# Kernel optimization log

Hardware: AMD Instinct MI355X
Metric: run time of the kernel (lower is better)

## Reference

```python
import jax, jax.numpy as jnp
import numpy as np

N_HEAD = 16
NUM_EXPERTS = 8
TOP_K = 2
LN_EPS = 1e-5


def setup_inputs() -> dict:
    key = jax.random.key(0)
    B, T, D = 8, 1024, 1024
    H = 4 * D
    E = NUM_EXPERTS
    ks = jax.random.split(key, 24)
    s = 0.02
    inp = {
        "x": jax.random.normal(ks[0], (B, T, D), jnp.float32),
        "ln1_g": jnp.ones((D,), jnp.float32),
        "ln1_b": jnp.zeros((D,), jnp.float32),
        "ln2_g": jnp.ones((D,), jnp.float32),
        "ln2_b": jnp.zeros((D,), jnp.float32),
        "Wq": jax.random.normal(ks[1], (D, D), jnp.float32) * s,
        "bq": jnp.zeros((D,), jnp.float32),
        "Wk": jax.random.normal(ks[2], (D, D), jnp.float32) * s,
        "bk": jnp.zeros((D,), jnp.float32),
        "Wv": jax.random.normal(ks[3], (D, D), jnp.float32) * s,
        "bv": jnp.zeros((D,), jnp.float32),
        "Wp": jax.random.normal(ks[4], (D, D), jnp.float32) * s,
        "bp": jnp.zeros((D,), jnp.float32),
        "gate_W": jax.random.normal(ks[5], (D, E), jnp.float32) * s,
        "gate_b": jnp.zeros((E,), jnp.float32),
        "exp_W1": jax.random.normal(ks[6], (E, D, H), jnp.float32) * s,
        "exp_b1": jnp.zeros((E, H), jnp.float32),
        "exp_W2": jax.random.normal(ks[7], (E, H, D), jnp.float32) * s,
        "exp_b2": jnp.zeros((E, D), jnp.float32),
    }
    return inp


def _layernorm(x, g, b):
    mu = jnp.mean(x, axis=-1, keepdims=True)
    var = jnp.mean(jnp.square(x - mu), axis=-1, keepdims=True)
    return (x - mu) * jax.lax.rsqrt(var + LN_EPS) * g + b


def _attention(h, Wq, bq, Wk, bk, Wv, bv, Wp, bp):
    B, T, D = h.shape
    hd = D // N_HEAD
    # [B,T,D] -> [B,Hh,T,hd]
    def split(z):
        return z.reshape(B, T, N_HEAD, hd).transpose(0, 2, 1, 3)
    q = split(h @ Wq + bq)
    k = split(h @ Wk + bk)
    v = split(h @ Wv + bv)
    att = jnp.einsum('bhqd,bhkd->bhqk', q, k) / jnp.sqrt(jnp.float32(hd))
    causal = jnp.tril(jnp.ones((T, T), bool))
    att = jnp.where(causal, att, -jnp.inf)
    att = jax.nn.softmax(att, axis=-1)
    y = jnp.einsum('bhqk,bhkd->bhqd', att, v)
    y = y.transpose(0, 2, 1, 3).reshape(B, T, D)
    return y @ Wp + bp


def _token_moe(h, gate_W, gate_b, exp_W1, exp_b1, exp_W2, exp_b2):
    B, T, D = h.shape
    flat = h.reshape(-1, D)                      # [N, D]
    N = flat.shape[0]
    logits = flat @ gate_W + gate_b              # [N, E]
    top_v, top_i = jax.lax.top_k(logits, TOP_K)  # [N, k]
    w = jax.nn.softmax(top_v, axis=-1)           # [N, k]
    # scatter top-k weights into dense [N, E] combine weights
    w_full = jnp.zeros((N, NUM_EXPERTS), flat.dtype)
    w_full = w_full.at[jnp.arange(N)[:, None], top_i].add(w)
    out = jnp.zeros_like(flat)
    for e in range(NUM_EXPERTS):  # small fixed expert count
        mid = jax.nn.gelu(flat @ exp_W1[e] + exp_b1[e], approximate=False)
        y_e = mid @ exp_W2[e] + exp_b2[e]
        out = out + w_full[:, e:e + 1] * y_e
    return out.reshape(B, T, D)


def reference(x, ln1_g, ln1_b, ln2_g, ln2_b, Wq, bq, Wk, bk, Wv, bv, Wp, bp,
              gate_W, gate_b, exp_W1, exp_b1, exp_W2, exp_b2):
    x = x + _attention(_layernorm(x, ln1_g, ln1_b), Wq, bq, Wk, bk, Wv, bv, Wp, bp)
    x = x + _token_moe(_layernorm(x, ln2_g, ln2_b), gate_W, gate_b,
                       exp_W1, exp_b1, exp_W2, exp_b2)
    return x
```

## Files before the change

kernel.cpp:

```cpp
#include <hip/hip_runtime.h>
#include <hip/hip_bf16.h>

#define D_MODEL 1024
#define H_MLP   4096
#define N_TOK   8192
#define T_SEQ   1024
#define NHEADS  16
#define HEAD_D  64
#define NEXPERT 8
#define LN_EPS  1e-5f
#define MAX_TILES 136
#define MAX_ROWS  (MAX_TILES * 128)
#define MB (1024 * 1024)

using f32x4 = __attribute__((ext_vector_type(4))) float;
using bh8   = __attribute__((ext_vector_type(8))) short;
typedef _Float16 h8 __attribute__((ext_vector_type(8)));

__device__ __forceinline__ unsigned short f2b(float f) {
  unsigned u = __float_as_uint(f);
  return (unsigned short)((u + 0x7FFFu + ((u >> 16) & 1u)) >> 16);
}
__device__ __forceinline__ float b2f(unsigned short h) {
  return __uint_as_float(((unsigned)h) << 16);
}
__device__ __forceinline__ void split16(float v, unsigned short& hi, unsigned short& lo) {
  const _Float16 h = (_Float16)v;
  const _Float16 l = (_Float16)(v - (float)h);
  hi = __builtin_bit_cast(unsigned short, h);
  lo = __builtin_bit_cast(unsigned short, l);
}
__device__ __forceinline__ void gll16(const unsigned short* g, unsigned short* lds) {
  __builtin_amdgcn_global_load_lds(
      (const __attribute__((address_space(1))) unsigned int*)(const void*)g,
      (__attribute__((address_space(3))) unsigned int*)(void*)lds, 16, 0, 0);
}

__global__ __launch_bounds__(256) void ln1_kernel(
    const float* __restrict__ x, const float* __restrict__ g,
    const float* __restrict__ b, unsigned short* __restrict__ oh,
    unsigned short* __restrict__ ol) {
  const int t = blockIdx.x, tid = threadIdx.x;
  const float4 v = ((const float4*)(x + (size_t)t * D_MODEL))[tid];
  float s  = v.x + v.y + v.z + v.w;
  float sq = v.x * v.x + v.y * v.y + v.z * v.z + v.w * v.w;
  __shared__ float red[8];
  #pragma unroll
  for (int o = 32; o > 0; o >>= 1) { s += __shfl_down(s, o); sq += __shfl_down(sq, o); }
  if ((tid & 63) == 0) { red[tid >> 6] = s; red[4 + (tid >> 6)] = sq; }
  __syncthreads();
  s  = red[0] + red[1] + red[2] + red[3];
  sq = red[4] + red[5] + red[6] + red[7];
  const float mu = s * (1.0f / D_MODEL);
  const float var = sq * (1.0f / D_MODEL) - mu * mu;
  const float rs = 1.0f / sqrtf(var + LN_EPS);
  const float4 gv = ((const float4*)g)[tid];
  const float4 bv = ((const float4*)b)[tid];
  float4 o;
  o.x = (v.x - mu) * rs * gv.x + bv.x;
  o.y = (v.y - mu) * rs * gv.y + bv.y;
  o.z = (v.z - mu) * rs * gv.z + bv.z;
  o.w = (v.w - mu) * rs * gv.w + bv.w;
  ushort4 hs, ls;
  split16(o.x, hs.x, ls.x); split16(o.y, hs.y, ls.y);
  split16(o.z, hs.z, ls.z); split16(o.w, hs.w, ls.w);
  ((ushort4*)(oh + (size_t)t * D_MODEL))[tid] = hs;
  ((ushort4*)(ol + (size_t)t * D_MODEL))[tid] = ls;
}

template<int MODE>
__global__ __launch_bounds__(256) void gemm_split_kernel(
    const unsigned short* __restrict__ Ah_g, const unsigned short* __restrict__ Al_g,
    const unsigned short* __restrict__ Bh_g, const unsigned short* __restrict__ Bl_g,
    const float* __restrict__ bias, const float* __restrict__ Rres,
    unsigned short* __restrict__ Ch, unsigned short* __restrict__ Cl,
    float* __restrict__ Cf, int M, int N, int K) {
  __shared__ unsigned short LAh[128 * 32], LAl[128 * 32];
  __shared__ unsigned short LBh[128 * 32], LBl[128 * 32];
  const int tid = threadIdx.x, lane = tid & 63, w = tid >> 6;
  const int bm = blockIdx.x * 128, bn = blockIdx.y * 128;
  const int wm = (w >> 1) * 64, wn = (w & 1) * 64;
  f32x4 acc[4][4];
  #pragma unroll
  for (int i = 0; i < 4; ++i)
    #pragma unroll
    for (int j = 0; j < 4; ++j) acc[i][j] = (f32x4){0.f, 0.f, 0.f, 0.f};
  const int lrow16 = lane >> 2, kq8 = (lane & 3) << 3;
  const int r0 = w * 16 + lrow16, r1 = 64 + w * 16 + lrow16;
  const size_t a0 = (size_t)(bm + r0) * K + kq8, a1 = (size_t)(bm + r1) * K + kq8;
  const size_t b0 = (size_t)(bn + r0) * K + kq8, b1 = (size_t)(bn + r1) * K + kq8;
  const int lb0 = (w * 16) * 32, lb1 = (64 + w * 16) * 32;
  const int lrow = lane & 15, lk = (lane >> 4) << 3;
  for (int k0 = 0; k0 < K; k0 += 32) {
    gll16(Ah_g + a0 + k0, &LAh[lb0]); gll16(Ah_g + a1 + k0, &LAh[lb1]);
    gll16(Al_g + a0 + k0, &LAl[lb0]); gll16(Al_g + a1 + k0, &LAl[lb1]);
    gll16(Bh_g + b0 + k0, &LBh[lb0]); gll16(Bh_g + b1 + k0, &LBh[lb1]);
    gll16(Bl_g + b0 + k0, &LBl[lb0]); gll16(Bl_g + b1 + k0, &LBl[lb1]);
    __syncthreads();
    h8 ah[4], al[4], bh[4], bl[4];
    #pragma unroll
    for (int i = 0; i < 4; ++i) {
      ah[i] = *(const h8*)&LAh[(wm + i * 16 + lrow) * 32 + lk];
      al[i] = *(const h8*)&LAl[(wm + i * 16 + lrow) * 32 + lk];
    }
    #pragma unroll
    for (int j = 0; j < 4; ++j) {
      bh[j] = *(const h8*)&LBh[(wn + j * 16 + lrow) * 32 + lk];
      bl[j] = *(const h8*)&LBl[(wn + j * 16 + lrow) * 32 + lk];
    }
    #pragma unroll
    for (int i = 0; i < 4; ++i)
      #pragma unroll
      for (int j = 0; j < 4; ++j) {
        acc[i][j] = __builtin_amdgcn_mfma_f32_16x16x32_f16(ah[i], bh[j], acc[i][j], 0, 0, 0);
        acc[i][j] = __builtin_amdgcn_mfma_f32_16x16x32_f16(ah[i], bl[j], acc[i][j], 0, 0, 0);
        acc[i][j] = __builtin_amdgcn_mfma_f32_16x16x32_f16(al[i], bh[j], acc[i][j], 0, 0, 0);
      }
    __syncthreads();
  }
  const int lc = lane & 15, lr4 = (lane >> 4) * 4;
  #pragma unroll
  for (int i = 0; i < 4; ++i)
    #pragma unroll
    for (int j = 0; j < 4; ++j) {
      const int col = bn + wn + j * 16 + lc;
      const float bsv = bias[col];
      #pragma unroll
      for (int qq = 0; qq < 4; ++qq) {
        const size_t row = (size_t)bm + wm + i * 16 + lr4 + qq;
        const size_t idx = row * N + col;
        const float v = acc[i][j][qq] + bsv;
        if (MODE == 0) {
          unsigned short hi, lo;
          split16(v, hi, lo);
          Ch[idx] = hi; Cl[idx] = lo;
        } else {
          Cf[idx] = v + Rres[idx];
        }
      }
    }
}

__global__ __launch_bounds__(256) void vtrans_kernel(
    const unsigned short* __restrict__ src, unsigned short* __restrict__ dst) {
  __shared__ unsigned short tile[64][72];
  const int tid = threadIdx.x;
  const int t0 = blockIdx.x * 64, bh = blockIdx.y;
  const int b = bh >> 4, h = bh & 15;
  #pragma unroll
  for (int it = 0; it < 2; ++it) {
    const int sg = tid + it * 256;
    const int r = sg >> 3, s = sg & 7;
    *(uint4*)&tile[r][s * 8] =
        *(const uint4*)(src + ((size_t)b * T_SEQ + t0 + r) * D_MODEL + h * HEAD_D + s * 8);
  }
  __syncthreads();
  #pragma unroll
  for (int it = 0; it < 2; ++it) {
    const int sg = tid + it * 256;
    const int d = sg >> 3, s = sg & 7;
    unsigned short v8[8] __attribute__((aligned(16)));
    #pragma unroll
    for (int j = 0; j < 8; ++j) v8[j] = tile[s * 8 + j][d];
    *(uint4*)(dst + ((size_t)bh * HEAD_D + d) * T_SEQ + t0 + s * 8) = *(const uint4*)v8;
  }
}

__global__ __launch_bounds__(256) void attn_mfma_kernel(
    const unsigned short* __restrict__ qh_g, const unsigned short* __restrict__ ql_g,
    const unsigned short* __restrict__ kh_g, const unsigned short* __restrict__ kl_g,
    const unsigned short* __restrict__ vth_g, const unsigned short* __restrict__ vtl_g,
    unsigned short* __restrict__ yh, unsigned short* __restrict__ yl) {
  __shared__ unsigned short Kh[64][72], Kl[64][72], Vh[64][72], Vl[64][72];
  __shared__ float Ps[4][16][68];
  const int tid = threadIdx.x, lane = tid & 63, w = tid >> 6;
  const int g = lane >> 4, c = lane & 15;
  const int qt = blockIdx.x, bh = blockIdx.y, b = bh >> 4, h = bh & 15;
  const size_t qrow0 = (size_t)b * T_SEQ + qt * 64;
  h8 aqh[2], aql[2];
  {
    const size_t rq = (qrow0 + w * 16 + c) * D_MODEL + h * HEAD_D + g * 8;
    aqh[0] = *(const h8*)(qh_g + rq);
    aqh[1] = *(const h8*)(qh_g + rq + 32);
    aql[0] = *(const h8*)(ql_g + rq);
    aql[1] = *(const h8*)(ql_g + rq + 32);
  }
  f32x4 oacc[4];
  #pragma unroll
  for (int i = 0; i < 4; ++i) oacc[i] = (f32x4){0.f, 0.f, 0.f, 0.f};
  float m[4] = {-3e38f, -3e38f, -3e38f, -3e38f};
  float l[4] = {0.f, 0.f, 0.f, 0.f};
  const int sgr = tid >> 3, sgs = tid & 7;
  for (int kt = 0; kt <= qt; ++kt) {
    const int kv0 = kt * 64;
    __syncthreads();
    {
      const size_t kb = ((size_t)b * T_SEQ + kv0) * D_MODEL + h * HEAD_D + sgs * 8;
      const size_t vb = (size_t)bh * HEAD_D * T_SEQ + kv0 + sgs * 8;
      *(uint4*)&Kh[sgr][sgs * 8]      = *(const uint4*)(kh_g + kb + (size_t)sgr * D_MODEL);
      *(uint4*)&Kh[sgr + 32][sgs * 8] = *(const uint4*)(kh_g + kb + (size_t)(sgr + 32) * D_MODEL);
      *(uint4*)&Kl[sgr][sgs * 8]      = *(const uint4*)(kl_g + kb + (size_t)sgr * D_MODEL);
      *(uint4*)&Kl[sgr + 32][sgs * 8] = *(const uint4*)(kl_g + kb + (size_t)(sgr + 32) * D_MODEL);
      *(uint4*)&Vh[sgr][sgs * 8]      = *(const uint4*)(vth_g + vb + (size_t)sgr * T_SEQ);
      *(uint4*)&Vh[sgr + 32][sgs * 8] = *(const uint4*)(vth_g + vb + (size_t)(sgr + 32) * T_SEQ);
      *(uint4*)&Vl[sgr][sgs * 8]      = *(const uint4*)(vtl_g + vb + (size_t)sgr * T_SEQ);
      *(uint4*)&Vl[sgr + 32][sgs * 8] = *(const uint4*)(vtl_g + vb + (size_t)(sgr + 32) * T_SEQ);
    }
    __syncthreads();
    f32x4 sv[4];
    #pragma unroll
    for (int nt = 0; nt < 4; ++nt) {
      f32x4 s = {0.f, 0.f, 0.f, 0.f};
      #pragma unroll
      for (int ks = 0; ks < 2; ++ks) {
        const h8 bkh = *(const h8*)&Kh[nt * 16 + c][ks * 32 + g * 8];
        const h8 bkl = *(const h8*)&Kl[nt * 16 + c][ks * 32 + g * 8];
        s = __builtin_amdgcn_mfma_f32_16x16x32_f16(aqh[ks], bkh, s, 0, 0, 0);
        s = __builtin_amdgcn_mfma_f32_16x16x32_f16(aqh[ks], bkl, s, 0, 0, 0);
        s = __builtin_amdgcn_mfma_f32_16x16x32_f16(aql[ks], bkh, s, 0, 0, 0);
      }
      sv[nt] = s;
    }
    float pm[4] = {-3e38f, -3e38f, -3e38f, -3e38f};
    #pragma unroll
    for (int nt = 0; nt < 4; ++nt)
      #pragma unroll
      for (int qq = 0; qq < 4; ++qq) {
        float sval = sv[nt][qq] * 0.125f;
        const int krow = kv0 + nt * 16 + c;
        const int qrow = qt * 64 + w * 16 + g * 4 + qq;
        sval = (krow <= qrow) ? sval : -3.0e38f;
        sv[nt][qq] = sval;
        pm[qq] = fmaxf(pm[qq], sval);
      }
    #pragma unroll
    for (int o = 1; o < 16; o <<= 1)
      #pragma unroll
      for (int qq = 0; qq < 4; ++qq) pm[qq] = fmaxf(pm[qq], __shfl_xor(pm[qq], o));
    float psum[4];
    #pragma unroll
    for (int qq = 0; qq < 4; ++qq) {
      const float mnew = fmaxf(m[qq], pm[qq]);
      const float sc = expf(m[qq] - mnew);
      m[qq] = mnew;
      l[qq] *= sc;
      #pragma unroll
      for (int dt = 0; dt < 4; ++dt) oacc[dt][qq] *= sc;
      psum[qq] = 0.f;
    }
    #pragma unroll
    for (int nt = 0; nt < 4; ++nt)
      #pragma unroll
      for (int qq = 0; qq < 4; ++qq) {
        const float p = expf(sv[nt][qq] - m[qq]);
        Ps[w][g * 4 + qq][nt * 16 + c] = p;
        psum[qq] += p;
      }
    #pragma unroll
    for (int o = 1; o < 16; o <<= 1)
      #pragma unroll
      for (int qq = 0; qq < 4; ++qq) psum[qq] += __shfl_xor(psum[qq], o);
    #pragma unroll
    for (int qq = 0; qq < 4; ++qq) l[qq] += psum[qq];
    #pragma unroll
    for (int ks = 0; ks < 2; ++ks) {
      const float4 p0 = *(const float4*)&Ps[w][c][ks * 32 + g * 8];
      const float4 p1 = *(const float4*)&Ps[w][c][ks * 32 + g * 8 + 4];
      const float pv[8] = {p0.x, p0.y, p0.z, p0.w, p1.x, p1.y, p1.z, p1.w};
      h8 pah, pal;
      #pragma unroll
      for (int j = 0; j < 8; ++j) {
        const _Float16 hi = (_Float16)pv[j];
        pah[j] = hi;
        pal[j] = (_Float16)(pv[j] - (float)hi);
      }
      #pragma unroll
      for (int dt = 0; dt < 4; ++dt) {
        const h8 bvh = *(const h8*)&Vh[dt * 16 + c][ks * 32 + g * 8];
        const h8 bvl = *(const h8*)&Vl[dt * 16 + c][ks * 32 + g * 8];
        oacc[dt] = __builtin_amdgcn_mfma_f32_16x16x32_f16(pah, bvh, oacc[dt], 0, 0, 0);
        oacc[dt] = __builtin_amdgcn_mfma_f32_16x16x32_f16(pah, bvl, oacc[dt], 0, 0, 0);
        oacc[dt] = __builtin_amdgcn_mfma_f32_16x16x32_f16(pal, bvh, oacc[dt], 0, 0, 0);
      }
    }
  }
  #pragma unroll
  for (int qq = 0; qq < 4; ++qq) {
    const float inv = 1.0f / l[qq];
    const size_t row = (qrow0 + w * 16 + g * 4 + qq) * D_MODEL + h * HEAD_D;
    #pragma unroll
    for (int dt = 0; dt < 4; ++dt) {
      unsigned short hi, lo;
      split16(oacc[dt][qq] * inv, hi, lo);
      yh[row + dt * 16 + c] = hi;
      yl[row + dt * 16 + c] = lo;
    }
  }
}

__global__ __launch_bounds__(256) void ln2_route_kernel(
    const float* __restrict__ x1, const float* __restrict__ g,
    const float* __restrict__ b, const float* __restrict__ gW,
    const float* __restrict__ gb, unsigned short* __restrict__ h2b,
    int2* __restrict__ tok_e, float2* __restrict__ tok_w, int* __restrict__ counts) {
  const int t = blockIdx.x, tid = threadIdx.x;
  const float4 v = ((const float4*)(x1 + (size_t)t * D_MODEL))[tid];
  float s  = v.x + v.y + v.z + v.w;
  float sq = v.x * v.x + v.y * v.y + v.z * v.z + v.w * v.w;
  __shared__ float red[8];
  __shared__ float lred[4][8];
  #pragma unroll
  for (int o = 32; o > 0; o >>= 1) { s += __shfl_down(s, o); sq += __shfl_down(sq, o); }
  if ((tid & 63) == 0) { red[tid >> 6] = s; red[4 + (tid >> 6)] = sq; }
  __syncthreads();
  s  = red[0] + red[1] + red[2] + red[3];
  sq = red[4] + red[5] + red[6] + red[7];
  const float mu = s * (1.0f / D_MODEL);
  const float var = sq * (1.0f / D_MODEL) - mu * mu;
  const float rs = 1.0f / sqrtf(var + LN_EPS);
  const float4 gv = ((const float4*)g)[tid];
  const float4 bv = ((const float4*)b)[tid];
  float4 hv;
  hv.x = (v.x - mu) * rs * gv.x + bv.x;
  hv.y = (v.y - mu) * rs * gv.y + bv.y;
  hv.z = (v.z - mu) * rs * gv.z + bv.z;
  hv.w = (v.w - mu) * rs * gv.w + bv.w;
  ushort4 hs;
  hs.x = f2b(hv.x); hs.y = f2b(hv.y); hs.z = f2b(hv.z); hs.w = f2b(hv.w);
  ((ushort4*)(h2b + (size_t)t * D_MODEL))[tid] = hs;
  float lg[8];
  const float* gwr = gW + (size_t)tid * 32;
  #pragma unroll
  for (int e = 0; e < 8; ++e)
    lg[e] = hv.x * gwr[e] + hv.y * gwr[8 + e] +
            hv.z * gwr[16 + e] + hv.w * gwr[24 + e];
  #pragma unroll
  for (int o = 32; o > 0; o >>= 1)
    #pragma unroll
    for (int e = 0; e < 8; ++e) lg[e] += __shfl_down(lg[e], o);
  if ((tid & 63) == 0)
    #pragma unroll
    for (int e = 0; e < 8; ++e) lred[tid >> 6][e] = lg[e];
  __syncthreads();
  if (tid == 0) {
    float L[8];
    #pragma unroll
    for (int e = 0; e < 8; ++e)
      L[e] = lred[0][e] + lred[1][e] + lred[2][e] + lred[3][e] + gb[e];
    int e0 = 0; float v0 = L[0];
    for (int e = 1; e < 8; ++e) if (L[e] > v0) { v0 = L[e]; e0 = e; }
    int e1 = (e0 == 0) ? 1 : 0; float v1 = L[e1];
    for (int e = 0; e < 8; ++e) if (e != e0 && L[e] > v1) { v1 = L[e]; e1 = e; }
    const float ew = expf(v1 - v0);
    const float inv = 1.0f / (1.0f + ew);
    tok_e[t] = make_int2(e0, e1);
    tok_w[t] = make_float2(inv, ew * inv);
    atomicAdd(&counts[e0], 1);
    atomicAdd(&counts[e1], 1);
  }
}

__global__ void route_offsets_kernel(const int* __restrict__ counts, int* __restrict__ off_al,
    int* __restrict__ ntiles, int* __restrict__ map_e, int* __restrict__ map_row) {
  if (threadIdx.x != 0 || blockIdx.x != 0) return;
  int off = 0, ti = 0;
  for (int e = 0; e < NEXPERT; ++e) {
    off_al[e] = off;
    const int tiles = (counts[e] + 127) >> 7;
    for (int j = 0; j < tiles; ++j) { map_e[ti] = e; map_row[ti] = off + (j << 7); ++ti; }
    off += tiles << 7;
  }
  off_al[NEXPERT] = off;
  ntiles[0] = ti;
}

__global__ __launch_bounds__(256) void place_kernel(
    const int2* __restrict__ tok_e, const int* __restrict__ off_al,
    int* __restrict__ cursors, int* __restrict__ list, int2* __restrict__ tok_pos) {
  const int t = blockIdx.x * 256 + threadIdx.x;
  if (t >= N_TOK) return;
  const int2 te = tok_e[t];
  const int p0 = off_al[te.x] + atomicAdd(&cursors[te.x], 1);
  const int p1 = off_al[te.y] + atomicAdd(&cursors[te.y], 1);
  list[p0] = t; list[p1] = t;
  tok_pos[t] = make_int2(p0, p1);
}

__global__ __launch_bounds__(256) void fill_pad_kernel(
    const int* __restrict__ counts, const int* __restrict__ off_al, int* __restrict__ list) {
  const int i = blockIdx.x * 256 + threadIdx.x;
  const int e = i >> 7, j = i & 127;
  if (e >= NEXPERT) return;
  const int start = off_al[e] + counts[e];
  if (start + j < off_al[e + 1]) list[start + j] = 0;
}

__global__ void transpose_cvt_kernel(
    const float* __restrict__ in, unsigned short* __restrict__ outp, int R, int C) {
  __shared__ float tile[32][33];
  const int e = blockIdx.z;
  const float* I = in + (size_t)e * R * C;
  unsigned short* O = outp + (size_t)e * R * C;
  const int c0 = blockIdx.x * 32, r0 = blockIdx.y * 32;
  const int tx = threadIdx.x, ty = threadIdx.y;
  #pragma unroll
  for (int j = 0; j < 32; j += 8)
    tile[ty + j][tx] = I[(size_t)(r0 + ty + j) * C + c0 + tx];
  __syncthreads();
  #pragma unroll
  for (int j = 0; j < 32; j += 8)
    O[(size_t)(c0 + ty + j) * R + r0 + tx] = f2b(tile[tx][ty + j]);
}

__global__ void transpose_cvt_f16_kernel(
    const float* __restrict__ in, unsigned short* __restrict__ oh,
    unsigned short* __restrict__ ol, int R, int C) {
  __shared__ float tile[32][33];
  const int c0 = blockIdx.x * 32, r0 = blockIdx.y * 32;
  const int tx = threadIdx.x, ty = threadIdx.y;
  #pragma unroll
  for (int j = 0; j < 32; j += 8)
    tile[ty + j][tx] = in[(size_t)(r0 + ty + j) * C + c0 + tx];
  __syncthreads();
  #pragma unroll
  for (int j = 0; j < 32; j += 8) {
    unsigned short hi, lo;
    split16(tile[tx][ty + j], hi, lo);
    oh[(size_t)(c0 + ty + j) * R + r0 + tx] = hi;
    ol[(size_t)(c0 + ty + j) * R + r0 + tx] = lo;
  }
}

template<int GELU_OUT, int GATHER>
__global__ __launch_bounds__(256) void moe_gemm_kernel(
    const unsigned short* __restrict__ Abase, const unsigned short* __restrict__ Bbase,
    const float* __restrict__ biasBase, unsigned short* __restrict__ midOut,
    float* __restrict__ fOut, const int* __restrict__ list,
    const int* __restrict__ map_e, const int* __restrict__ map_row,
    const int* __restrict__ ntiles_p, int K, int N) {
  const int mt = blockIdx.x;
  if (mt >= ntiles_p[0]) return;
  const int e = map_e[mt];
  const int row0 = map_row[mt];
  const int bn = blockIdx.y * 128;
  const unsigned short* Bp = Bbase + (size_t)e * (size_t)N * (size_t)K;
  const float* bias = biasBase + (size_t)e * N;
  __shared__ unsigned short As[128 * 32];
  __shared__ unsigned short Bs[128 * 32];
  const int tid = threadIdx.x, lane = tid & 63, wid = tid >> 6;
  const int wm = (wid >> 1) * 64, wn = (wid & 1) * 64;
  f32x4 acc[4][4];
  #pragma unroll
  for (int i = 0; i < 4; ++i)
    #pragma unroll
    for (int j = 0; j < 4; ++j) acc[i][j] = (f32x4){0.f, 0.f, 0.f, 0.f};
  const int lrow16 = lane >> 2, kq8 = (lane & 3) << 3;
  const int r0 = wid * 16 + lrow16, r1 = 64 + wid * 16 + lrow16;
  size_t arow0, arow1;
  if (GATHER) {
    arow0 = (size_t)list[row0 + r0] * (size_t)K + kq8;
    arow1 = (size_t)list[row0 + r1] * (size_t)K + kq8;
  } else {
    arow0 = (size_t)(row0 + r0) * (size_t)K + kq8;
    arow1 = (size_t)(row0 + r1) * (size_t)K + kq8;
  }
  const size_t brow0 = (size_t)(bn + r0) * (size_t)K + kq8;
  const size_t brow1 = (size_t)(bn + r1) * (size_t)K + kq8;
  const int lb0 = (wid * 16) * 32, lb1 = (64 + wid * 16) * 32;
  const int lrow = lane & 15, lk = (lane >> 4) << 3;
  for (int k0 = 0; k0 < K; k0 += 32) {
    gll16(Abase + arow0 + k0, &As[lb0]);
    gll16(Abase + arow1 + k0, &As[lb1]);
    gll16(Bp + brow0 + k0, &Bs[lb0]);
    gll16(Bp + brow1 + k0, &Bs[lb1]);
    __syncthreads();
    bh8 a[4], b[4];
    #pragma unroll
    for (int i = 0; i < 4; ++i) a[i] = *(const bh8*)&As[(wm + i * 16 + lrow) * 32 + lk];
    #pragma unroll
    for (int j = 0; j < 4; ++j) b[j] = *(const bh8*)&Bs[(wn + j * 16 + lrow) * 32 + lk];
    #pragma unroll
    for (int i = 0; i < 4; ++i)
      #pragma unroll
      for (int j = 0; j < 4; ++j)
        acc[i][j] = __builtin_amdgcn_mfma_f32_16x16x32_bf16(a[i], b[j], acc[i][j], 0, 0, 0);
    __syncthreads();
  }
  const int lc = lane & 15, lr4 = (lane >> 4) * 4;
  #pragma unroll
  for (int i = 0; i < 4; ++i)
    #pragma unroll
    for (int j = 0; j < 4; ++j) {
      const int col = bn + wn + j * 16 + lc;
      const float bsv = bias[col];
      #pragma unroll
      for (int qq = 0; qq < 4; ++qq) {
        const int rowl = wm + i * 16 + lr4 + qq;
        const size_t idx = (size_t)(row0 + rowl) * N + col;
        const float xv = acc[i][j][qq] + bsv;
        if (GELU_OUT) {
          const float gel = 0.5f * xv * (1.0f + erff(xv * 0.70710678118654752f));
          midOut[idx] = f2b(gel);
        } else {
          fOut[idx] = xv;
        }
      }
    }
}

__global__ __launch_bounds__(256) void combine_kernel(
    const float* __restrict__ x1, const float* __restrict__ ylist,
    const int2* __restrict__ tok_pos, const float2* __restrict__ tok_w,
    float* __restrict__ outp) {
  const int t = blockIdx.x, tid = threadIdx.x;
  const int2 p = tok_pos[t];
  const float2 w = tok_w[t];
  const float4 a  = ((const float4*)(x1 + (size_t)t * D_MODEL))[tid];
  const float4 y0 = ((const float4*)(ylist + (size_t)p.x * D_MODEL))[tid];
  const float4 y1 = ((const float4*)(ylist + (size_t)p.y * D_MODEL))[tid];
  float4 o;
  o.x = a.x + w.x * y0.x + w.y * y1.x;
  o.y = a.y + w.x * y0.y + w.y * y1.y;
  o.z = a.z + w.x * y0.z + w.y * y1.z;
  o.w = a.w + w.x * y0.w + w.y * y1.w;
  ((float4*)(outp + (size_t)t * D_MODEL))[tid] = o;
}

extern "C" void kernel_launch(void* const* d_in, const int* in_sizes, int n_in,
                              void* d_out, int out_size, void* d_ws, size_t ws_size,
                              hipStream_t stream) {
  const float* x    = (const float*)d_in[0];
  const float* ln1g = (const float*)d_in[1];
  const float* ln1b = (const float*)d_in[2];
  const float* ln2g = (const float*)d_in[3];
  const float* ln2b = (const float*)d_in[4];
  const float* Wq   = (const float*)d_in[5];
  const float* bq   = (const float*)d_in[6];
  const float* Wk   = (const float*)d_in[7];
  const float* bk   = (const float*)d_in[8];
  const float* Wv   = (const float*)d_in[9];
  const float* bv   = (const float*)d_in[10];
  const float* Wp   = (const float*)d_in[11];
  const float* bp   = (const float*)d_in[12];
  const float* gW   = (const float*)d_in[13];
  const float* gb   = (const float*)d_in[14];
  const float* eW1  = (const float*)d_in[15];
  const float* eb1  = (const float*)d_in[16];
  const float* eW2  = (const float*)d_in[17];
  const float* eb2  = (const float*)d_in[18];
  float* out = (float*)d_out;
  (void)in_sizes; (void)n_in; (void)out_size;

  char* wsb = (char*)d_ws;
  size_t off = 0;
  auto alloc = [&](size_t bytes) -> void* {
    void* p = wsb + off;
    off += (bytes + 255) & ~(size_t)255;
    return p;
  };
  int*  counts  = (int*)alloc(32);
  int*  cursors = (int*)alloc(32);
  int*  off_al  = (int*)alloc(64);
  int*  ntiles  = (int*)alloc(64);
  int*  map_e   = (int*)alloc(MAX_TILES * 4);
  int*  map_row = (int*)alloc(MAX_TILES * 4);
  const size_t ctrl_bytes = off;
  int2*   tok_e   = (int2*)alloc((size_t)N_TOK * 8);
  float2* tok_w   = (float2*)alloc((size_t)N_TOK * 8);
  int2*   tok_pos = (int2*)alloc((size_t)N_TOK * 8);
  int*    list    = (int*)alloc((size_t)MAX_ROWS * 4);
  float* x1  = (float*)alloc((size_t)N_TOK * D_MODEL * 4);
  unsigned short* h2b = (unsigned short*)alloc((size_t)N_TOK * D_MODEL * 2);
  unsigned short* W1T = (unsigned short*)alloc((size_t)NEXPERT * D_MODEL * H_MLP * 2);
  unsigned short* W2T = (unsigned short*)alloc((size_t)NEXPERT * D_MODEL * H_MLP * 2);
  float* ylist = (float*)alloc((size_t)MAX_ROWS * D_MODEL * 4);
  unsigned short* WqTh = (unsigned short*)alloc((size_t)D_MODEL * D_MODEL * 2);
  unsigned short* WqTl = (unsigned short*)alloc((size_t)D_MODEL * D_MODEL * 2);
  unsigned short* WkTh = (unsigned short*)alloc((size_t)D_MODEL * D_MODEL * 2);
  unsigned short* WkTl = (unsigned short*)alloc((size_t)D_MODEL * D_MODEL * 2);
  unsigned short* WvTh = (unsigned short*)alloc((size_t)D_MODEL * D_MODEL * 2);
  unsigned short* WvTl = (unsigned short*)alloc((size_t)D_MODEL * D_MODEL * 2);
  unsigned short* WpTh = (unsigned short*)alloc((size_t)D_MODEL * D_MODEL * 2);
  unsigned short* WpTl = (unsigned short*)alloc((size_t)D_MODEL * D_MODEL * 2);
  char* arena = (char*)alloc((size_t)160 * MB);
  unsigned short* h1h = (unsigned short*)(arena);
  unsigned short* h1l = (unsigned short*)(arena + (size_t) 16 * MB);
  unsigned short* qh_ = (unsigned short*)(arena + (size_t) 32 * MB);
  unsigned short* ql_ = (unsigned short*)(arena + (size_t) 48 * MB);
  unsigned short* kh_ = (unsigned short*)(arena + (size_t) 64 * MB);
  unsigned short* kl_ = (unsigned short*)(arena + (size_t) 80 * MB);
  unsigned short* vh_ = (unsigned short*)(arena + (size_t) 96 * MB);
  unsigned short* vl_ = (unsigned short*)(arena + (size_t)112 * MB);
  unsigned short* vth_ = (unsigned short*)(arena + (size_t)128 * MB);
  unsigned short* vtl_ = (unsigned short*)(arena + (size_t)144 * MB);
  unsigned short* yh_ = vh_;
  unsigned short* yl_ = vl_;
  unsigned short* mid = (unsigned short*)(arena);
  if (off > ws_size) return;

  hipMemsetAsync(d_ws, 0, ctrl_bytes, stream);

  transpose_cvt_kernel<<<dim3(H_MLP / 32, D_MODEL / 32, NEXPERT), dim3(32, 8), 0, stream>>>(
      eW1, W1T, D_MODEL, H_MLP);
  transpose_cvt_kernel<<<dim3(D_MODEL / 32, H_MLP / 32, NEXPERT), dim3(32, 8), 0, stream>>>(
      eW2, W2T, H_MLP, D_MODEL);
  transpose_cvt_f16_kernel<<<dim3(32, 32), dim3(32, 8), 0, stream>>>(Wq, WqTh, WqTl, D_MODEL, D_MODEL);
  transpose_cvt_f16_kernel<<<dim3(32, 32), dim3(32, 8), 0, stream>>>(Wk, WkTh, WkTl, D_MODEL, D_MODEL);
  transpose_cvt_f16_kernel<<<dim3(32, 32), dim3(32, 8), 0, stream>>>(Wv, WvTh, WvTl, D_MODEL, D_MODEL);
  transpose_cvt_f16_kernel<<<dim3(32, 32), dim3(32, 8), 0, stream>>>(Wp, WpTh, WpTl, D_MODEL, D_MODEL);

  ln1_kernel<<<N_TOK, 256, 0, stream>>>(x, ln1g, ln1b, h1h, h1l);

  gemm_split_kernel<0><<<dim3(64, 8), 256, 0, stream>>>(
      h1h, h1l, WqTh, WqTl, bq, nullptr, qh_, ql_, nullptr, N_TOK, D_MODEL, D_MODEL);
  gemm_split_kernel<0><<<dim3(64, 8), 256, 0, stream>>>(
      h1h, h1l, WkTh, WkTl, bk, nullptr, kh_, kl_, nullptr, N_TOK, D_MODEL, D_MODEL);
  gemm_split_kernel<0><<<dim3(64, 8), 256, 0, stream>>>(
      h1h, h1l, WvTh, WvTl, bv, nullptr, vh_, vl_, nullptr, N_TOK, D_MODEL, D_MODEL);

  vtrans_kernel<<<dim3(T_SEQ / 64, (N_TOK / T_SEQ) * NHEADS), 256, 0, stream>>>(vh_, vth_);
  vtrans_kernel<<<dim3(T_SEQ / 64, (N_TOK / T_SEQ) * NHEADS), 256, 0, stream>>>(vl_, vtl_);

  attn_mfma_kernel<<<dim3(T_SEQ / 64, (N_TOK / T_SEQ) * NHEADS), 256, 0, stream>>>(
      qh_, ql_, kh_, kl_, vth_, vtl_, yh_, yl_);

  gemm_split_kernel<1><<<dim3(64, 8), 256, 0, stream>>>(
      yh_, yl_, WpTh, WpTl, bp, x, nullptr, nullptr, x1, N_TOK, D_MODEL, D_MODEL);

  ln2_route_kernel<<<N_TOK, 256, 0, stream>>>(x1, ln2g, ln2b, gW, gb, h2b, tok_e, tok_w, counts);
  route_offsets_kernel<<<1, 64, 0, stream>>>(counts, off_al, ntiles, map_e, map_row);
  place_kernel<<<N_TOK / 256, 256, 0, stream>>>(tok_e, off_al, cursors, list, tok_pos);
  fill_pad_kernel<<<4, 256, 0, stream>>>(counts, off_al, list);

  moe_gemm_kernel<1, 1><<<dim3(MAX_TILES, H_MLP / 128), 256, 0, stream>>>(
      h2b, W1T, eb1, mid, nullptr, list, map_e, map_row, ntiles, D_MODEL, H_MLP);
  moe_gemm_kernel<0, 0><<<dim3(MAX_TILES, D_MODEL / 128), 256, 0, stream>>>(
      mid, W2T, eb2, nullptr, ylist, list, map_e, map_row, ntiles, H_MLP, D_MODEL);

  combine_kernel<<<N_TOK, 256, 0, stream>>>(x1, ylist, tok_pos, tok_w, out);
}
```

Before: 1.469 ms.

## Enlarge attention query tile to 128 rows with 8 waves and reverse tile order

The attention kernel now gives each block 128 query rows and 8 waves, so every K/V tile loaded into shared memory serves twice as many queries and per-thread load work halves. Blocks are launched in reverse query-tile order so the longest causal blocks start first, which should even out the tail. The P scratch buffer is halved and refilled per 32-column half, and s_setprio raises wave priority around the MFMA sections. The risks are lower occupancy from larger blocks, fewer blocks in the grid, and the upper-half waves doing masked work on the last key tile.

```diff
diff --git a/kernel.cpp b/kernel.cpp
--- a/kernel.cpp
+++ b/kernel.cpp
@@ -166,17 +166,18 @@
   }
 }
 
-__global__ __launch_bounds__(256) void attn_mfma_kernel(
+__global__ __launch_bounds__(512) void attn_mfma_kernel(
     const unsigned short* __restrict__ qh_g, const unsigned short* __restrict__ ql_g,
     const unsigned short* __restrict__ kh_g, const unsigned short* __restrict__ kl_g,
     const unsigned short* __restrict__ vth_g, const unsigned short* __restrict__ vtl_g,
     unsigned short* __restrict__ yh, unsigned short* __restrict__ yl) {
   __shared__ unsigned short Kh[64][72], Kl[64][72], Vh[64][72], Vl[64][72];
-  __shared__ float Ps[4][16][68];
+  __shared__ float Ps[8][16][36];
   const int tid = threadIdx.x, lane = tid & 63, w = tid >> 6;
   const int g = lane >> 4, c = lane & 15;
-  const int qt = blockIdx.x, bh = blockIdx.y, b = bh >> 4, h = bh & 15;
-  const size_t qrow0 = (size_t)b * T_SEQ + qt * 64;
+  const int qt = (int)gridDim.x - 1 - (int)blockIdx.x;
+  const int bh = blockIdx.y, b = bh >> 4, h = bh & 15;
+  const size_t qrow0 = (size_t)b * T_SEQ + qt * 128;
   h8 aqh[2], aql[2];
   {
     const size_t rq = (qrow0 + w * 16 + c) * D_MODEL + h * HEAD_D + g * 8;
@@ -191,23 +192,21 @@
   float m[4] = {-3e38f, -3e38f, -3e38f, -3e38f};
   float l[4] = {0.f, 0.f, 0.f, 0.f};
   const int sgr = tid >> 3, sgs = tid & 7;
-  for (int kt = 0; kt <= qt; ++kt) {
+  const int nkt = 2 * qt + 2;
+  for (int kt = 0; kt < nkt; ++kt) {
     const int kv0 = kt * 64;
     __syncthreads();
     {
-      const size_t kb = ((size_t)b * T_SEQ + kv0) * D_MODEL + h * HEAD_D + sgs * 8;
-      const size_t vb = (size_t)bh * HEAD_D * T_SEQ + kv0 + sgs * 8;
-      *(uint4*)&Kh[sgr][sgs * 8]      = *(const uint4*)(kh_g + kb + (size_t)sgr * D_MODEL);
-      *(uint4*)&Kh[sgr + 32][sgs * 8] = *(const uint4*)(kh_g + kb + (size_t)(sgr + 32) * D_MODEL);
-      *(uint4*)&Kl[sgr][sgs * 8]      = *(const uint4*)(kl_g + kb + (size_t)sgr * D_MODEL);
-      *(uint4*)&Kl[sgr + 32][sgs * 8] = *(const uint4*)(kl_g + kb + (size_t)(sgr + 32) * D_MODEL);
-      *(uint4*)&Vh[sgr][sgs * 8]      = *(const uint4*)(vth_g + vb + (size_t)sgr * T_SEQ);
-      *(uint4*)&Vh[sgr + 32][sgs * 8] = *(const uint4*)(vth_g + vb + (size_t)(sgr + 32) * T_SEQ);
-      *(uint4*)&Vl[sgr][sgs * 8]      = *(const uint4*)(vtl_g + vb + (size_t)sgr * T_SEQ);
-      *(uint4*)&Vl[sgr + 32][sgs * 8] = *(const uint4*)(vtl_g + vb + (size_t)(sgr + 32) * T_SEQ);
+      const size_t kb = ((size_t)b * T_SEQ + kv0 + sgr) * D_MODEL + h * HEAD_D + sgs * 8;
+      const size_t vb = ((size_t)bh * HEAD_D + sgr) * T_SEQ + kv0 + sgs * 8;
+      *(uint4*)&Kh[sgr][sgs * 8] = *(const uint4*)(kh_g + kb);
+      *(uint4*)&Kl[sgr][sgs * 8] = *(const uint4*)(kl_g + kb);
+      *(uint4*)&Vh[sgr][sgs * 8] = *(const uint4*)(vth_g + vb);
+      *(uint4*)&Vl[sgr][sgs * 8] = *(const uint4*)(vtl_g + vb);
     }
     __syncthreads();
     f32x4 sv[4];
+    __builtin_amdgcn_s_setprio(1);
     #pragma unroll
     for (int nt = 0; nt < 4; ++nt) {
       f32x4 s = {0.f, 0.f, 0.f, 0.f};
@@ -221,6 +220,7 @@
       }
       sv[nt] = s;
     }
+    __builtin_amdgcn_s_setprio(0);
     float pm[4] = {-3e38f, -3e38f, -3e38f, -3e38f};
     #pragma unroll
     for (int nt = 0; nt < 4; ++nt)
@@ -228,7 +228,7 @@
       for (int qq = 0; qq < 4; ++qq) {
         float sval = sv[nt][qq] * 0.125f;
         const int krow = kv0 + nt * 16 + c;
-        const int qrow = qt * 64 + w * 16 + g * 4 + qq;
+        const int qrow = qt * 128 + w * 16 + g * 4 + qq;
         sval = (krow <= qrow) ? sval : -3.0e38f;
         sv[nt][qq] = sval;
         pm[qq] = fmaxf(pm[qq], sval);
@@ -253,7 +253,7 @@
       #pragma unroll
       for (int qq = 0; qq < 4; ++qq) {
         const float p = expf(sv[nt][qq] - m[qq]);
-        Ps[w][g * 4 + qq][nt * 16 + c] = p;
+        sv[nt][qq] = p;
         psum[qq] += p;
       }
     #pragma unroll
@@ -263,9 +263,14 @@
     #pragma unroll
     for (int qq = 0; qq < 4; ++qq) l[qq] += psum[qq];
     #pragma unroll
-    for (int ks = 0; ks < 2; ++ks) {
-      const float4 p0 = *(const float4*)&Ps[w][c][ks * 32 + g * 8];
-      const float4 p1 = *(const float4*)&Ps[w][c][ks * 32 + g * 8 + 4];
+    for (int half = 0; half < 2; ++half) {
+      #pragma unroll
+      for (int nt2 = 0; nt2 < 2; ++nt2)
+        #pragma unroll
+        for (int qq = 0; qq < 4; ++qq)
+          Ps[w][g * 4 + qq][nt2 * 16 + c] = sv[half * 2 + nt2][qq];
+      const float4 p0 = *(const float4*)&Ps[w][c][g * 8];
+      const float4 p1 = *(const float4*)&Ps[w][c][g * 8 + 4];
       const float pv[8] = {p0.x, p0.y, p0.z, p0.w, p1.x, p1.y, p1.z, p1.w};
       h8 pah, pal;
       #pragma unroll
@@ -274,14 +279,17 @@
         pah[j] = hi;
         pal[j] = (_Float16)(pv[j] - (float)hi);
       }
+      __builtin_amdgcn_s_setprio(1);
       #pragma unroll
       for (int dt = 0; dt < 4; ++dt) {
-        const h8 bvh = *(const h8*)&Vh[dt * 16 + c][ks * 32 + g * 8];
-        const h8 bvl = *(const h8*)&Vl[dt * 16 + c][ks * 32 + g * 8];
+        const h8 bvh = *(const h8*)&Vh[dt * 16 + c][half * 32 + g * 8];
+        const h8 bvl = *(const h8*)&Vl[dt * 16 + c][half * 32 + g * 8];
         oacc[dt] = __builtin_amdgcn_mfma_f32_16x16x32_f16(pah, bvh, oacc[dt], 0, 0, 0);
         oacc[dt] = __builtin_amdgcn_mfma_f32_16x16x32_f16(pah, bvl, oacc[dt], 0, 0, 0);
         oacc[dt] = __builtin_amdgcn_mfma_f32_16x16x32_f16(pal, bvh, oacc[dt], 0, 0, 0);
       }
+      __builtin_amdgcn_s_setprio(0);
+      if (half == 0) __builtin_amdgcn_sched_barrier(0);
     }
   }
   #pragma unroll
@@ -621,7 +629,7 @@
   vtrans_kernel<<<dim3(T_SEQ / 64, (N_TOK / T_SEQ) * NHEADS), 256, 0, stream>>>(vh_, vth_);
   vtrans_kernel<<<dim3(T_SEQ / 64, (N_TOK / T_SEQ) * NHEADS), 256, 0, stream>>>(vl_, vtl_);
 
-  attn_mfma_kernel<<<dim3(T_SEQ / 64, (N_TOK / T_SEQ) * NHEADS), 256, 0, stream>>>(
+  attn_mfma_kernel<<<dim3(T_SEQ / 128, (N_TOK / T_SEQ) * NHEADS), 512, 0, stream>>>(
       qh_, ql_, kh_, kl_, vth_, vtl_, yh_, yl_);
 
   gemm_split_kernel<1><<<dim3(64, 8), 256, 0, stream>>>(
```

Result: faster. 1.324 ms (-9.8%).
